# Kernel tuning notes

Hardware: AMD Instinct MI355X
Metric: run time of the kernel (lower is better)

## Reference

```python
import math
import jax, jax.numpy as jnp
import numpy as np

L, D, H, DFF, T, B, BUCKETS = 4, 512, 8, 2048, 256, 8, 32
DH = D // H


def _ln(x, g, b, eps=1e-6):
    m = x.mean(-1, keepdims=True)
    v = ((x - m) ** 2).mean(-1, keepdims=True)
    return (x - m) / jnp.sqrt(v + eps) * g + b


def setup_inputs() -> dict:
    key = jax.random.key(0)
    ki = iter(jax.random.split(key, 32))
    p = lambda shape: jax.random.normal(next(ki), shape, jnp.float32) * 0.02
    inp = {}
    inp['src'] = jax.random.normal(next(ki), (T, B, D), jnp.float32)
    inp['lengths'] = jax.random.randint(next(ki), (B,), 128, T + 1)
    inp['distances'] = jax.random.randint(next(ki), (B, T, T), 0, BUCKETS + 1)
    inp['u'] = jax.random.normal(next(ki), (D,), jnp.float32)
    inp['v'] = jax.random.normal(next(ki), (D,), jnp.float32)
    inp['ln1_g'] = jnp.ones((L, D)); inp['ln1_b'] = jnp.zeros((L, D))
    for nm in ['Wq', 'Wk', 'Wv', 'Wo']:
        inp[nm] = p((L, D, D))
    for nm in ['bq', 'bk', 'bv', 'bo']:
        inp[nm] = jnp.zeros((L, D))
    # learned relative-position embedding table per layer, padding row zeroed
    inp['rel_table'] = p((L, BUCKETS + 1, D)).at[:, BUCKETS, :].set(0.0)
    inp['ffn_ln_g'] = jnp.ones((L, D)); inp['ffn_ln_b'] = jnp.zeros((L, D))
    inp['W1'] = p((L, DFF, D)); inp['b1'] = jnp.zeros((L, DFF))
    inp['W2'] = p((L, D, DFF)); inp['b2'] = jnp.zeros((L, D))
    inp['final_ln_g'] = jnp.ones((D,)); inp['final_ln_b'] = jnp.zeros((D,))
    return inp


def reference(src, lengths, distances, u, v, ln1_g, ln1_b, Wq, bq, Wk, bk, Wv, bv,
              Wo, bo, rel_table, ffn_ln_g, ffn_ln_b, W1, b1, W2, b2,
              final_ln_g, final_ln_b):
    # onmt-style sinusoidal positional encoding with sqrt(d_model) scaling
    pos = jnp.arange(T, dtype=jnp.float32)[:, None]
    div = jnp.exp(jnp.arange(0, D, 2, dtype=jnp.float32) * (-math.log(10000.0) / D))
    pe = jnp.zeros((T, D)).at[:, 0::2].set(jnp.sin(pos * div)).at[:, 1::2].set(jnp.cos(pos * div))
    x = (src * math.sqrt(D) + pe[:, None, :]).transpose(1, 0, 2)  # (B,T,D)
    pad = jnp.arange(T)[None, :] >= lengths[:, None]  # (B,T), True = masked key
    uh = u.reshape(1, H, 1, DH)
    vh = v.reshape(1, H, 1, DH)
    for l in range(L):
        h = _ln(x, ln1_g[l], ln1_b[l])
        def heads(w, b_):
            return (h @ w.T + b_).reshape(B, T, H, DH).transpose(0, 2, 1, 3)
        q = heads(Wq[l], bq[l]) / math.sqrt(DH)  # (B,H,T,DH)
        k = heads(Wk[l], bk[l])
        val = heads(Wv[l], bv[l])
        # content term a_c = (q + u) k^T
        a_c = jnp.einsum('bhqd,bhkd->bhqk', q + uh, k)
        # relative term b_d = (q + v) R^T, R gathered per (query,key) pair
        rel = rel_table[l][distances].reshape(B, T, T, H, DH)  # (B,Q,K,H,DH)
        b_d = jnp.einsum('bhqd,bqkhd->bhqk', q + vh, rel)
        scores = (a_c + b_d).astype(jnp.float32)
        scores = jnp.where(pad[:, None, None, :], -1e18, scores)
        attn = jax.nn.softmax(scores, axis=-1)
        ctx = jnp.einsum('bhqk,bhkd->bhqd', attn, val)
        ctx = ctx.transpose(0, 2, 1, 3).reshape(B, T, D)
        out = ctx @ Wo[l].T + bo[l] + x  # residual (dropout=0)
        # PositionwiseFeedForward: LN -> W1 -> relu -> W2 -> +residual
        h2 = _ln(out, ffn_ln_g[l], ffn_ln_b[l])
        x = jax.nn.relu(h2 @ W1[l].T + b1[l]) @ W2[l].T + b2[l] + out
    x = _ln(x, final_ln_g, final_ln_b)
    return x.transpose(1, 0, 2)  # (T,B,D)
```

## Files before the change

### kernel.cpp

```cpp
#include <hip/hip_runtime.h>
#include <hip/hip_bf16.h>
#include <math.h>

constexpr int L = 4, D = 512, H = 8, DFF = 2048, T = 256, B = 8, BUCKETS = 32;
constexpr int DH = D / H;
constexpr int NT = B * T;
constexpr int QKVLD = 3 * D;

typedef __attribute__((ext_vector_type(8))) short bf16x8;
typedef __attribute__((ext_vector_type(4))) float f32x4;

__device__ __forceinline__ unsigned short f2bf(float f) {
    unsigned int x = __float_as_uint(f);
    return (unsigned short)((x + 0x7fffu + ((x >> 16) & 1u)) >> 16);
}
__device__ __forceinline__ float bf2f(unsigned short u) {
    return __uint_as_float((unsigned int)u << 16);
}

__device__ __forceinline__ void stage16(const unsigned short* g, short* l) {
    __builtin_amdgcn_global_load_lds((const __attribute__((address_space(1))) unsigned int*)g,
                                     (__attribute__((address_space(3))) unsigned int*)l,
                                     16, 0, 0);
}

__global__ __launch_bounds__(256) void embed_kernel(const float* __restrict__ src,
                                                    float* __restrict__ x)
{
    int t = blockIdx.x, tid = threadIdx.x;
    float pe0, pe1;
    {
        int d0 = tid, d1 = tid + 256;
        float dv0 = expf(-(float)(2 * (d0 >> 1)) * (9.210340371976184f / (float)D));
        float dv1 = expf(-(float)(2 * (d1 >> 1)) * (9.210340371976184f / (float)D));
        float a0 = (float)t * dv0, a1 = (float)t * dv1;
        pe0 = (d0 & 1) ? cosf(a0) : sinf(a0);
        pe1 = (d1 & 1) ? cosf(a1) : sinf(a1);
    }
#pragma unroll
    for (int b = 0; b < B; b++) {
        const float* sp = src + ((size_t)t * B + b) * D;
        float* xp = x + ((size_t)(b * T + t)) * D;
        xp[tid]       = sp[tid]       * 22.62741699796952f + pe0;
        xp[tid + 256] = sp[tid + 256] * 22.62741699796952f + pe1;
    }
}

__device__ __forceinline__ void ln_vals(float v0, float v1,
                                        const float* __restrict__ g,
                                        const float* __restrict__ bb,
                                        float* o0, float* o1, int tid)
{
    float s = v0 + v1, q2 = v0 * v0 + v1 * v1;
#pragma unroll
    for (int o = 32; o; o >>= 1) { s += __shfl_xor(s, o); q2 += __shfl_xor(q2, o); }
    __shared__ float rs[4], rq[4];
    int lane = tid & 63, wid = tid >> 6;
    if (lane == 0) { rs[wid] = s; rq[wid] = q2; }
    __syncthreads();
    s = rs[0] + rs[1] + rs[2] + rs[3];
    q2 = rq[0] + rq[1] + rq[2] + rq[3];
    float mean = s * (1.f / (float)D);
    float var = q2 * (1.f / (float)D) - mean * mean;
    float rstd = rsqrtf(var + 1e-6f);
    *o0 = (v0 - mean) * rstd * g[tid] + bb[tid];
    *o1 = (v1 - mean) * rstd * g[tid + 256] + bb[tid + 256];
}

__global__ __launch_bounds__(256) void ln_kernel(const float* __restrict__ x,
                                                 unsigned short* __restrict__ y,
                                                 const float* __restrict__ g,
                                                 const float* __restrict__ bb)
{
    int row = blockIdx.x, tid = threadIdx.x;
    float v0 = x[(size_t)row * D + tid], v1 = x[(size_t)row * D + tid + 256];
    float o0, o1;
    ln_vals(v0, v1, g, bb, &o0, &o1, tid);
    y[(size_t)row * D + tid] = f2bf(o0);
    y[(size_t)row * D + tid + 256] = f2bf(o1);
}

__global__ __launch_bounds__(256) void lnr_kernel(float* __restrict__ X,
                                                  const float* __restrict__ P,
                                                  const float* __restrict__ bias,
                                                  unsigned short* __restrict__ y,
                                                  const float* __restrict__ g,
                                                  const float* __restrict__ bb)
{
    int row = blockIdx.x, tid = threadIdx.x;
    float v0 = X[(size_t)row * D + tid] + bias[tid];
    float v1 = X[(size_t)row * D + tid + 256] + bias[tid + 256];
#pragma unroll
    for (int s = 0; s < 4; s++) {
        v0 += P[((size_t)s * NT + row) * D + tid];
        v1 += P[((size_t)s * NT + row) * D + tid + 256];
    }
    X[(size_t)row * D + tid] = v0;
    X[(size_t)row * D + tid + 256] = v1;
    float o0, o1;
    ln_vals(v0, v1, g, bb, &o0, &o1, tid);
    y[(size_t)row * D + tid] = f2bf(o0);
    y[(size_t)row * D + tid + 256] = f2bf(o1);
}

__global__ __launch_bounds__(256) void final_lnr_kernel(const float* __restrict__ X,
                                                        const float* __restrict__ P,
                                                        const float* __restrict__ bias,
                                                        float* __restrict__ out,
                                                        const float* __restrict__ g,
                                                        const float* __restrict__ bb)
{
    int row = blockIdx.x, tid = threadIdx.x;
    int b = row >> 8, t = row & (T - 1);
    float v0 = X[(size_t)row * D + tid] + bias[tid];
    float v1 = X[(size_t)row * D + tid + 256] + bias[tid + 256];
#pragma unroll
    for (int s = 0; s < 4; s++) {
        v0 += P[((size_t)s * NT + row) * D + tid];
        v1 += P[((size_t)s * NT + row) * D + tid + 256];
    }
    float o0, o1;
    ln_vals(v0, v1, g, bb, &o0, &o1, tid);
    float* op = out + ((size_t)t * B + b) * D;
    op[tid] = o0;
    op[tid + 256] = o1;
}

__global__ __launch_bounds__(256) void convert_all_kernel(
    const float* __restrict__ Wq, const float* __restrict__ Wk, const float* __restrict__ Wv,
    const float* __restrict__ Wo, const float* __restrict__ W1, const float* __restrict__ W2,
    const float* __restrict__ bq, const float* __restrict__ bk, const float* __restrict__ bv,
    const float* __restrict__ rel,
    unsigned short* __restrict__ WQKVb, unsigned short* __restrict__ Wob,
    unsigned short* __restrict__ W1b, unsigned short* __restrict__ W2b,
    unsigned short* __restrict__ relb,
    float* __restrict__ bqkv)
{
    int l = blockIdx.y;
    int g = blockIdx.x * 256 + threadIdx.x;
    const float* src; unsigned short* dst;
    bool zero = false;
    if (g < 98304) {
        int e = g * 8; int piece = e >> 18; int rem = e & 262143;
        src = (piece == 0 ? Wq : piece == 1 ? Wk : Wv) + (size_t)l * 262144 + rem;
        dst = WQKVb + (size_t)l * 786432 + e;
    } else if (g < 131072) {
        int e = (g - 98304) * 8;
        src = Wo + (size_t)l * 262144 + e; dst = Wob + (size_t)l * 262144 + e;
    } else if (g < 262144) {
        int e = (g - 131072) * 8;
        src = W1 + (size_t)l * 1048576 + e; dst = W1b + (size_t)l * 1048576 + e;
    } else if (g < 393216) {
        int e = (g - 262144) * 8;
        src = W2 + (size_t)l * 1048576 + e; dst = W2b + (size_t)l * 1048576 + e;
    } else {
        int e = (g - 393216) * 8;
        int row = e >> 9, cc = e & 511;
        dst = relb + (size_t)l * 24576 + e;
        if (row < BUCKETS + 1) src = rel + ((size_t)l * (BUCKETS + 1) + row) * 512 + cc;
        else { src = nullptr; zero = true; }
    }
    uint4 o;
    if (zero) { o.x = o.y = o.z = o.w = 0u; }
    else {
        float4 x = *(const float4*)src, y = *(const float4*)(src + 4);
        o.x = (unsigned)f2bf(x.x) | ((unsigned)f2bf(x.y) << 16);
        o.y = (unsigned)f2bf(x.z) | ((unsigned)f2bf(x.w) << 16);
        o.z = (unsigned)f2bf(y.x) | ((unsigned)f2bf(y.y) << 16);
        o.w = (unsigned)f2bf(y.z) | ((unsigned)f2bf(y.w) << 16);
    }
    *(uint4*)dst = o;
    if (g < 3 * D) {
        int piece = g >> 9, r2 = g & 511;
        bqkv[l * 1536 + g] = (piece == 0 ? bq : piece == 1 ? bk : bv)[l * 512 + r2];
    }
}

template <bool RELU, bool OUTBF16>
__global__ __launch_bounds__(256) void mgemm_kernel(
    const unsigned short* __restrict__ A,
    const unsigned short* __restrict__ W,
    const float* __restrict__ bias,
    void* __restrict__ Cv,
    int N, int M, int K)
{
    __shared__ short smA[2][128 * 32];
    __shared__ short smB[2][128 * 32];
    int tid = threadIdx.x;
    int bn = blockIdx.y * 128;
    int bm = blockIdx.x * 128;
    const unsigned short* Ab = A + (size_t)bn * K;
    const unsigned short* Wb = W + (size_t)bm * K;

    f32x4 acc[4][4];
#pragma unroll
    for (int i = 0; i < 4; i++)
#pragma unroll
        for (int j = 0; j < 4; j++) acc[i][j] = (f32x4){0.f, 0.f, 0.f, 0.f};

    const int c0 = tid, c1 = tid + 256;
    const int r0 = c0 >> 2, p0 = c0 & 3, l0 = p0 ^ ((r0 >> 1) & 3);
    const int r1 = c1 >> 2, p1 = c1 & 3, l1 = p1 ^ ((r1 >> 1) & 3);

    auto stage = [&](int buf, int k0) {
        stage16(Ab + (size_t)r0 * K + k0 + l0 * 8, &smA[buf][c0 * 8]);
        stage16(Ab + (size_t)r1 * K + k0 + l1 * 8, &smA[buf][c1 * 8]);
        stage16(Wb + (size_t)r0 * K + k0 + l0 * 8, &smB[buf][c0 * 8]);
        stage16(Wb + (size_t)r1 * K + k0 + l1 * 8, &smB[buf][c1 * 8]);
    };

    const int lane = tid & 63;
    const int wv = tid >> 6, wr = wv >> 1, wc = wv & 1;
    int aoff[4], boff[4];
#pragma unroll
    for (int i = 0; i < 4; i++) {
        int ra = wr * 64 + i * 16 + (lane & 15);
        int ca = (lane >> 4) ^ ((ra >> 1) & 3);
        aoff[i] = ra * 32 + ca * 8;
        int rb = wc * 64 + i * 16 + (lane & 15);
        int cb = (lane >> 4) ^ ((rb >> 1) & 3);
        boff[i] = rb * 32 + cb * 8;
    }

    stage(0, 0);
    const int nkt = K >> 5;
    for (int kt = 0; kt < nkt; ++kt) {
        __syncthreads();
        int cur = kt & 1;
        if (kt + 1 < nkt) stage(cur ^ 1, (kt + 1) << 5);
        const short* sa = smA[cur];
        const short* sb = smB[cur];
        bf16x8 af[4], bfr[4];
#pragma unroll
        for (int i = 0; i < 4; i++) af[i] = *(const bf16x8*)(sa + aoff[i]);
#pragma unroll
        for (int j = 0; j < 4; j++) bfr[j] = *(const bf16x8*)(sb + boff[j]);
#pragma unroll
        for (int i = 0; i < 4; i++)
#pragma unroll
            for (int j = 0; j < 4; j++)
                acc[i][j] = __builtin_amdgcn_mfma_f32_16x16x32_bf16(af[i], bfr[j], acc[i][j], 0, 0, 0);
    }

#pragma unroll
    for (int j = 0; j < 4; j++) {
        int col = bm + wc * 64 + j * 16 + (lane & 15);
        float bval = bias[col];
#pragma unroll
        for (int i = 0; i < 4; i++) {
            f32x4 v = acc[i][j];
#pragma unroll
            for (int r = 0; r < 4; r++) {
                int row = bn + wr * 64 + i * 16 + (lane >> 4) * 4 + r;
                float val = v[r] + bval;
                if (RELU) val = fmaxf(val, 0.f);
                if (OUTBF16) ((unsigned short*)Cv)[(size_t)row * M + col] = f2bf(val);
                else         ((float*)Cv)[(size_t)row * M + col] = val;
            }
        }
    }
}

__global__ __launch_bounds__(256) void mgemm_splitk_kernel(
    const unsigned short* __restrict__ A,
    const unsigned short* __restrict__ W,
    float* __restrict__ P,
    int N, int M, int K, int Ksub)
{
    __shared__ short smA[2][128 * 32];
    __shared__ short smB[2][128 * 32];
    int tid = threadIdx.x;
    int s = blockIdx.z;
    int bn = blockIdx.y * 128;
    int bm = blockIdx.x * 128;
    const unsigned short* Ab = A + (size_t)bn * K + s * Ksub;
    const unsigned short* Wb = W + (size_t)bm * K + s * Ksub;

    f32x4 acc[4][4];
#pragma unroll
    for (int i = 0; i < 4; i++)
#pragma unroll
        for (int j = 0; j < 4; j++) acc[i][j] = (f32x4){0.f, 0.f, 0.f, 0.f};

    const int c0 = tid, c1 = tid + 256;
    const int r0 = c0 >> 2, p0 = c0 & 3, l0 = p0 ^ ((r0 >> 1) & 3);
    const int r1 = c1 >> 2, p1 = c1 & 3, l1 = p1 ^ ((r1 >> 1) & 3);

    auto stage = [&](int buf, int k0) {
        stage16(Ab + (size_t)r0 * K + k0 + l0 * 8, &smA[buf][c0 * 8]);
        stage16(Ab + (size_t)r1 * K + k0 + l1 * 8, &smA[buf][c1 * 8]);
        stage16(Wb + (size_t)r0 * K + k0 + l0 * 8, &smB[buf][c0 * 8]);
        stage16(Wb + (size_t)r1 * K + k0 + l1 * 8, &smB[buf][c1 * 8]);
    };

    const int lane = tid & 63;
    const int wv = tid >> 6, wr = wv >> 1, wc = wv & 1;
    int aoff[4], boff[4];
#pragma unroll
    for (int i = 0; i < 4; i++) {
        int ra = wr * 64 + i * 16 + (lane & 15);
        int ca = (lane >> 4) ^ ((ra >> 1) & 3);
        aoff[i] = ra * 32 + ca * 8;
        int rb = wc * 64 + i * 16 + (lane & 15);
        int cb = (lane >> 4) ^ ((rb >> 1) & 3);
        boff[i] = rb * 32 + cb * 8;
    }

    stage(0, 0);
    const int nkt = Ksub >> 5;
    for (int kt = 0; kt < nkt; ++kt) {
        __syncthreads();
        int cur = kt & 1;
        if (kt + 1 < nkt) stage(cur ^ 1, (kt + 1) << 5);
        const short* sa = smA[cur];
        const short* sb = smB[cur];
        bf16x8 af[4], bfr[4];
#pragma unroll
        for (int i = 0; i < 4; i++) af[i] = *(const bf16x8*)(sa + aoff[i]);
#pragma unroll
        for (int j = 0; j < 4; j++) bfr[j] = *(const bf16x8*)(sb + boff[j]);
#pragma unroll
        for (int i = 0; i < 4; i++)
#pragma unroll
            for (int j = 0; j < 4; j++)
                acc[i][j] = __builtin_amdgcn_mfma_f32_16x16x32_bf16(af[i], bfr[j], acc[i][j], 0, 0, 0);
    }

#pragma unroll
    for (int j = 0; j < 4; j++) {
        int col = bm + wc * 64 + j * 16 + (lane & 15);
#pragma unroll
        for (int i = 0; i < 4; i++) {
            f32x4 v = acc[i][j];
#pragma unroll
            for (int r = 0; r < 4; r++) {
                int row = bn + wr * 64 + i * 16 + (lane >> 4) * 4 + r;
                P[((size_t)s * N + row) * M + col] = v[r];
            }
        }
    }
}

__global__ __launch_bounds__(256) void vtrans_kernel(const unsigned short* __restrict__ qkv,
                                                     unsigned short* __restrict__ vt)
{
    __shared__ unsigned short tile[64 * 66];
    int bh = blockIdx.x, b = bh >> 3, h = bh & 7;
    int kc = blockIdx.y * 64;
    int tid = threadIdx.x;
    int r = tid >> 2, c0 = (tid & 3) * 16;
    const unsigned short* rp = qkv + (size_t)(b * T + kc + r) * QKVLD + 2 * D + h * 64 + c0;
    uint4 w0 = *(const uint4*)rp;
    uint4 w1 = *(const uint4*)(rp + 8);
    unsigned short* tp = &tile[r * 66 + c0];
    unsigned int ww[8] = {w0.x, w0.y, w0.z, w0.w, w1.x, w1.y, w1.z, w1.w};
#pragma unroll
    for (int e = 0; e < 8; e++) {
        tp[2 * e]     = (unsigned short)(ww[e] & 0xffffu);
        tp[2 * e + 1] = (unsigned short)(ww[e] >> 16);
    }
    __syncthreads();
    int d = tid >> 2, k0 = (tid & 3) * 16;
    unsigned int outw[8];
#pragma unroll
    for (int i = 0; i < 8; i++) {
        unsigned int lo = tile[(k0 + 2 * i) * 66 + d];
        unsigned int hi = tile[(k0 + 2 * i + 1) * 66 + d];
        outw[i] = lo | (hi << 16);
    }
    unsigned short* op = vt + (size_t)(bh * 64 + d) * 256 + kc + k0;
    *(uint4*)op = *(uint4*)&outw[0];
    *(uint4*)(op + 8) = *(uint4*)&outw[4];
}

__global__ __launch_bounds__(256) void fattn_kernel(
    const unsigned short* __restrict__ qkv,
    const unsigned short* __restrict__ vt,
    const unsigned short* __restrict__ relb,
    const float* __restrict__ uvec,
    const float* __restrict__ vvec,
    const int* __restrict__ dist,
    const int* __restrict__ lengths,
    unsigned short* __restrict__ ctx)
{
    __shared__ unsigned short Ps[4][16][256];
    __shared__ float Qrel[4][16][49];

    int bh = blockIdx.x, b = bh >> 3, h = bh & 7;
    int qi0 = blockIdx.y * 64;
    int tid = threadIdx.x, w = tid >> 6, lane = tid & 63;
    int l15 = lane & 15, g = lane >> 4;
    int qr = qi0 + w * 16;

    const unsigned short* qbase = qkv + (size_t)(b * T + qr + l15) * QKVLD + h * 64 + g * 8;
    bf16x8 qa0 = *(const bf16x8*)(qbase);
    bf16x8 qa1 = *(const bf16x8*)(qbase + 32);

    bf16x8 qu0, qu1;
    {
        const float* up = uvec + h * 64 + g * 8;
        float ua0[8], ua1[8];
        *(float4*)&ua0[0] = *(const float4*)(up);
        *(float4*)&ua0[4] = *(const float4*)(up + 4);
        *(float4*)&ua1[0] = *(const float4*)(up + 32);
        *(float4*)&ua1[4] = *(const float4*)(up + 36);
#pragma unroll
        for (int e = 0; e < 8; e++) {
            qu0[e] = (short)f2bf(0.125f * bf2f((unsigned short)qa0[e]) + ua0[e]);
            qu1[e] = (short)f2bf(0.125f * bf2f((unsigned short)qa1[e]) + ua1[e]);
        }
    }

    {
        const float* vp = vvec + h * 64 + g * 8;
        float va0[8], va1[8];
        *(float4*)&va0[0] = *(const float4*)(vp);
        *(float4*)&va0[4] = *(const float4*)(vp + 4);
        *(float4*)&va1[0] = *(const float4*)(vp + 32);
        *(float4*)&va1[4] = *(const float4*)(vp + 36);
        bf16x8 qh0, qh1;
#pragma unroll
        for (int e = 0; e < 8; e++) {
            qh0[e] = (short)f2bf(0.125f * bf2f((unsigned short)qa0[e]) + va0[e]);
            qh1[e] = (short)f2bf(0.125f * bf2f((unsigned short)qa1[e]) + va1[e]);
        }
        f32x4 qacc[3];
#pragma unroll
        for (int j = 0; j < 3; j++) qacc[j] = (f32x4){0.f, 0.f, 0.f, 0.f};
#pragma unroll
        for (int j = 0; j < 3; j++) {
            const unsigned short* rp = relb + (size_t)(j * 16 + l15) * 512 + h * 64 + g * 8;
            bf16x8 r0 = *(const bf16x8*)(rp);
            bf16x8 r1 = *(const bf16x8*)(rp + 32);
            qacc[j] = __builtin_amdgcn_mfma_f32_16x16x32_bf16(qh0, r0, qacc[j], 0, 0, 0);
            qacc[j] = __builtin_amdgcn_mfma_f32_16x16x32_bf16(qh1, r1, qacc[j], 0, 0, 0);
        }
#pragma unroll
        for (int j = 0; j < 3; j++)
#pragma unroll
            for (int r = 0; r < 4; r++)
                Qrel[w][g * 4 + r][j * 16 + l15] = qacc[j][r];
    }

    f32x4 acc[16];
#pragma unroll
    for (int j = 0; j < 16; j++) acc[j] = (f32x4){0.f, 0.f, 0.f, 0.f};
    const unsigned short* kbase = qkv + (size_t)(b * T) * QKVLD + 512 + h * 64 + g * 8;
#pragma unroll
    for (int j = 0; j < 16; j++) {
        const unsigned short* kp = kbase + (size_t)(j * 16 + l15) * QKVLD;
        bf16x8 k0 = *(const bf16x8*)(kp);
        bf16x8 k1 = *(const bf16x8*)(kp + 32);
        acc[j] = __builtin_amdgcn_mfma_f32_16x16x32_bf16(qu0, k0, acc[j], 0, 0, 0);
        acc[j] = __builtin_amdgcn_mfma_f32_16x16x32_bf16(qu1, k1, acc[j], 0, 0, 0);
    }

    int len = lengths[b];
    float rinv[4];
    const int* db = dist + (size_t)b * T * T;
#pragma unroll
    for (int r = 0; r < 4; r++) {
        int rowloc = g * 4 + r;
        int qrow = qr + rowloc;
        const int* dpr = db + (size_t)qrow * T;
        float m = -3.0e38f;
#pragma unroll
        for (int j = 0; j < 16; j++) {
            int ki = j * 16 + l15;
            int dv = dpr[ki];
            float s = acc[j][r] + Qrel[w][rowloc][dv];
            s = (ki < len) ? s : -1.0e30f;
            acc[j][r] = s;
            m = fmaxf(m, s);
        }
#pragma unroll
        for (int o = 8; o; o >>= 1) m = fmaxf(m, __shfl_xor(m, o));
        float sum = 0.f;
#pragma unroll
        for (int j = 0; j < 16; j++) {
            int ki = j * 16 + l15;
            float p = __expf(acc[j][r] - m);
            sum += p;
            int cph = ((ki >> 3) ^ (rowloc & 7));
            Ps[w][rowloc][cph * 8 + (ki & 7)] = f2bf(p);
        }
#pragma unroll
        for (int o = 8; o; o >>= 1) sum += __shfl_xor(sum, o);
        rinv[r] = 1.0f / sum;
    }

    f32x4 oacc[4];
#pragma unroll
    for (int j = 0; j < 4; j++) oacc[j] = (f32x4){0.f, 0.f, 0.f, 0.f};
    const unsigned short* vtb = vt + (size_t)bh * 64 * 256;
#pragma unroll
    for (int ks = 0; ks < 8; ks++) {
        int c = ks * 4 + g;
        int cph = c ^ (l15 & 7);
        bf16x8 pa = *(const bf16x8*)&Ps[w][l15][cph * 8];
#pragma unroll
        for (int j2 = 0; j2 < 4; j2++) {
            bf16x8 vb = *(const bf16x8*)(vtb + (size_t)(j2 * 16 + l15) * 256 + c * 8);
            oacc[j2] = __builtin_amdgcn_mfma_f32_16x16x32_bf16(pa, vb, oacc[j2], 0, 0, 0);
        }
    }

#pragma unroll
    for (int j2 = 0; j2 < 4; j2++) {
#pragma unroll
        for (int r = 0; r < 4; r++) {
            int qrow = qr + g * 4 + r;
            int dcol = j2 * 16 + l15;
            ctx[(size_t)(b * T + qrow) * D + h * 64 + dcol] = f2bf(oacc[j2][r] * rinv[r]);
        }
    }
}

extern "C" void kernel_launch(void* const* d_in, const int* in_sizes, int n_in,
                              void* d_out, int out_size, void* d_ws, size_t ws_size,
                              hipStream_t stream)
{
    const float* src     = (const float*)d_in[0];
    const int*   lengths = (const int*)d_in[1];
    const int*   dist    = (const int*)d_in[2];
    const float* u       = (const float*)d_in[3];
    const float* v       = (const float*)d_in[4];
    const float* ln1_g   = (const float*)d_in[5];
    const float* ln1_b   = (const float*)d_in[6];
    const float* Wq      = (const float*)d_in[7];
    const float* Wk      = (const float*)d_in[8];
    const float* Wv      = (const float*)d_in[9];
    const float* Wo      = (const float*)d_in[10];
    const float* bq      = (const float*)d_in[11];
    const float* bk      = (const float*)d_in[12];
    const float* bv      = (const float*)d_in[13];
    const float* bo      = (const float*)d_in[14];
    const float* rel     = (const float*)d_in[15];
    const float* fg      = (const float*)d_in[16];
    const float* fb      = (const float*)d_in[17];
    const float* W1      = (const float*)d_in[18];
    const float* b1      = (const float*)d_in[19];
    const float* W2      = (const float*)d_in[20];
    const float* b2      = (const float*)d_in[21];
    const float* flg     = (const float*)d_in[22];
    const float* flb     = (const float*)d_in[23];

    float* ws = (float*)d_ws;
    float*          X     = ws;
    unsigned short* QKVb  = (unsigned short*)(ws + 1048576);
    unsigned short* Hb    = (unsigned short*)(ws + 2621440);
    unsigned short* CTX   = (unsigned short*)(ws + 3145728);
    unsigned short* FF1   = (unsigned short*)(ws + 3670016);
    unsigned short* VT    = (unsigned short*)(ws + 5767168);
    float*          Pbuf  = ws + 6291456;
    unsigned short* WQKVb = (unsigned short*)(ws + 10485760);
    unsigned short* Wob   = (unsigned short*)(ws + 12058624);
    unsigned short* W1b   = (unsigned short*)(ws + 12582912);
    unsigned short* W2b   = (unsigned short*)(ws + 14680064);
    unsigned short* RELb  = (unsigned short*)(ws + 16777216);
    float*          bqkv  = ws + 16826368;

    embed_kernel<<<T, 256, 0, stream>>>(src, X);

    convert_all_kernel<<<dim3(1548, L), 256, 0, stream>>>(
        Wq, Wk, Wv, Wo, W1, W2, bq, bk, bv, rel,
        WQKVb, Wob, W1b, W2b, RELb, bqkv);

    for (int l = 0; l < L; l++) {
        const unsigned short* wqkv = WQKVb + (size_t)l * 786432;
        const unsigned short* wob  = Wob   + (size_t)l * 262144;
        const unsigned short* w1b  = W1b   + (size_t)l * 1048576;
        const unsigned short* w2b  = W2b   + (size_t)l * 1048576;
        const unsigned short* relb = RELb  + (size_t)l * 24576;
        const float*          bql  = bqkv  + (size_t)l * 1536;

        if (l == 0)
            ln_kernel<<<NT, 256, 0, stream>>>(X, Hb, ln1_g, ln1_b);
        else
            lnr_kernel<<<NT, 256, 0, stream>>>(X, Pbuf, b2 + (size_t)(l - 1) * D,
                                               Hb, ln1_g + l * D, ln1_b + l * D);

        mgemm_kernel<false, true><<<dim3(12, 16), 256, 0, stream>>>(
            Hb, wqkv, bql, QKVb, NT, QKVLD, D);

        vtrans_kernel<<<dim3(64, 4), 256, 0, stream>>>(QKVb, VT);

        fattn_kernel<<<dim3(B * H, T / 64), 256, 0, stream>>>(
            QKVb, VT, relb, u, v, dist, lengths, CTX);

        mgemm_splitk_kernel<<<dim3(4, 16, 4), 256, 0, stream>>>(
            CTX, wob, Pbuf, NT, D, D, D / 4);

        lnr_kernel<<<NT, 256, 0, stream>>>(X, Pbuf, bo + (size_t)l * D,
                                           Hb, fg + l * D, fb + l * D);

        mgemm_kernel<true, true><<<dim3(16, 16), 256, 0, stream>>>(
            Hb, w1b, b1 + (size_t)l * DFF, FF1, NT, DFF, D);

        mgemm_splitk_kernel<<<dim3(4, 16, 4), 256, 0, stream>>>(
            FF1, w2b, Pbuf, NT, D, DFF, DFF / 4);
    }

    final_lnr_kernel<<<NT, 256, 0, stream>>>(X, Pbuf, b2 + (size_t)(L - 1) * D,
                                             (float*)d_out, flg, flb);
}
```

Measured before the change: 521.8 us.

## Fuse embedding into first LayerNorm and write transposed V from QKV GEMM epilogue

Merges the positional-embedding kernel into the first LayerNorm so the embedded activations are computed, stored and normalised in one pass, dropping a kernel launch and a reread of X. The QKV GEMM epilogue also writes the V columns directly in the transposed per-head layout used by attention, which removes the separate vtrans kernel and its extra read of QKV. In exchange the embed kernel now recomputes sin/cos per row and the GEMM epilogue performs scattered 8-byte transposed stores. The split-K store index was also changed from N to NT, which gives the same value at the existing call sites.

```diff
diff --git a/kernel.cpp b/kernel.cpp
--- a/kernel.cpp
+++ b/kernel.cpp
@@ -24,32 +24,10 @@
                                      16, 0, 0);
 }
 
-__global__ __launch_bounds__(256) void embed_kernel(const float* __restrict__ src,
-                                                    float* __restrict__ x)
-{
-    int t = blockIdx.x, tid = threadIdx.x;
-    float pe0, pe1;
-    {
-        int d0 = tid, d1 = tid + 256;
-        float dv0 = expf(-(float)(2 * (d0 >> 1)) * (9.210340371976184f / (float)D));
-        float dv1 = expf(-(float)(2 * (d1 >> 1)) * (9.210340371976184f / (float)D));
-        float a0 = (float)t * dv0, a1 = (float)t * dv1;
-        pe0 = (d0 & 1) ? cosf(a0) : sinf(a0);
-        pe1 = (d1 & 1) ? cosf(a1) : sinf(a1);
-    }
-#pragma unroll
-    for (int b = 0; b < B; b++) {
-        const float* sp = src + ((size_t)t * B + b) * D;
-        float* xp = x + ((size_t)(b * T + t)) * D;
-        xp[tid]       = sp[tid]       * 22.62741699796952f + pe0;
-        xp[tid + 256] = sp[tid + 256] * 22.62741699796952f + pe1;
-    }
-}
-
-__device__ __forceinline__ void ln_vals(float v0, float v1,
-                                        const float* __restrict__ g,
-                                        const float* __restrict__ bb,
-                                        float* o0, float* o1, int tid)
+__device__ __forceinline__ void ln_vals_k(float v0, float v1,
+                                          const float* __restrict__ g,
+                                          const float* __restrict__ bb,
+                                          float* o0, float* o1, int tid)
 {
     float s = v0 + v1, q2 = v0 * v0 + v1 * v1;
 #pragma unroll
@@ -67,17 +45,29 @@
     *o1 = (v1 - mean) * rstd * g[tid + 256] + bb[tid + 256];
 }
 
-__global__ __launch_bounds__(256) void ln_kernel(const float* __restrict__ x,
-                                                 unsigned short* __restrict__ y,
-                                                 const float* __restrict__ g,
-                                                 const float* __restrict__ bb)
+__global__ __launch_bounds__(256) void embed_ln_kernel(const float* __restrict__ src,
+                                                       float* __restrict__ X,
+                                                       unsigned short* __restrict__ Hb,
+                                                       const float* __restrict__ g,
+                                                       const float* __restrict__ bb)
 {
     int row = blockIdx.x, tid = threadIdx.x;
-    float v0 = x[(size_t)row * D + tid], v1 = x[(size_t)row * D + tid + 256];
+    int b = row >> 8, t = row & (T - 1);
+    int d0 = tid, d1 = tid + 256;
+    float dv0 = expf(-(float)(2 * (d0 >> 1)) * (9.210340371976184f / (float)D));
+    float dv1 = expf(-(float)(2 * (d1 >> 1)) * (9.210340371976184f / (float)D));
+    float a0 = (float)t * dv0, a1 = (float)t * dv1;
+    float pe0 = (d0 & 1) ? cosf(a0) : sinf(a0);
+    float pe1 = (d1 & 1) ? cosf(a1) : sinf(a1);
+    const float* sp = src + ((size_t)t * B + b) * D;
+    float v0 = sp[d0] * 22.62741699796952f + pe0;
+    float v1 = sp[d1] * 22.62741699796952f + pe1;
+    X[(size_t)row * D + d0] = v0;
+    X[(size_t)row * D + d1] = v1;
     float o0, o1;
-    ln_vals(v0, v1, g, bb, &o0, &o1, tid);
-    y[(size_t)row * D + tid] = f2bf(o0);
-    y[(size_t)row * D + tid + 256] = f2bf(o1);
+    ln_vals_k(v0, v1, g, bb, &o0, &o1, tid);
+    Hb[(size_t)row * D + d0] = f2bf(o0);
+    Hb[(size_t)row * D + d1] = f2bf(o1);
 }
 
 __global__ __launch_bounds__(256) void lnr_kernel(float* __restrict__ X,
@@ -98,7 +88,7 @@
     X[(size_t)row * D + tid] = v0;
     X[(size_t)row * D + tid + 256] = v1;
     float o0, o1;
-    ln_vals(v0, v1, g, bb, &o0, &o1, tid);
+    ln_vals_k(v0, v1, g, bb, &o0, &o1, tid);
     y[(size_t)row * D + tid] = f2bf(o0);
     y[(size_t)row * D + tid + 256] = f2bf(o1);
 }
@@ -120,7 +110,7 @@
         v1 += P[((size_t)s * NT + row) * D + tid + 256];
     }
     float o0, o1;
-    ln_vals(v0, v1, g, bb, &o0, &o1, tid);
+    ln_vals_k(v0, v1, g, bb, &o0, &o1, tid);
     float* op = out + ((size_t)t * B + b) * D;
     op[tid] = o0;
     op[tid + 256] = o1;
@@ -176,12 +166,13 @@
     }
 }
 
-template <bool RELU, bool OUTBF16>
+template <bool RELU, bool OUTBF16, bool VTOUT>
 __global__ __launch_bounds__(256) void mgemm_kernel(
     const unsigned short* __restrict__ A,
     const unsigned short* __restrict__ W,
     const float* __restrict__ bias,
     void* __restrict__ Cv,
+    unsigned short* __restrict__ vt,
     int N, int M, int K)
 {
     __shared__ short smA[2][128 * 32];
@@ -249,13 +240,24 @@
 #pragma unroll
         for (int i = 0; i < 4; i++) {
             f32x4 v = acc[i][j];
+            int row0 = bn + wr * 64 + i * 16 + (lane >> 4) * 4;
+            unsigned short ob[4];
 #pragma unroll
             for (int r = 0; r < 4; r++) {
-                int row = bn + wr * 64 + i * 16 + (lane >> 4) * 4 + r;
                 float val = v[r] + bval;
                 if (RELU) val = fmaxf(val, 0.f);
-                if (OUTBF16) ((unsigned short*)Cv)[(size_t)row * M + col] = f2bf(val);
-                else         ((float*)Cv)[(size_t)row * M + col] = val;
+                unsigned short bfv = f2bf(val);
+                ob[r] = bfv;
+                if (OUTBF16) ((unsigned short*)Cv)[(size_t)(row0 + r) * M + col] = bfv;
+                else         ((float*)Cv)[(size_t)(row0 + r) * M + col] = val;
+            }
+            if (VTOUT && col >= 1024) {
+                int d = col - 1024;
+                int b = row0 >> 8, ki = row0 & (T - 1);
+                uint2 pk;
+                pk.x = (unsigned)ob[0] | ((unsigned)ob[1] << 16);
+                pk.y = (unsigned)ob[2] | ((unsigned)ob[3] << 16);
+                *(uint2*)(vt + ((size_t)(b * H + (d >> 6)) * 64 + (d & 63)) * 256 + ki) = pk;
             }
         }
     }
@@ -335,42 +337,10 @@
 #pragma unroll
             for (int r = 0; r < 4; r++) {
                 int row = bn + wr * 64 + i * 16 + (lane >> 4) * 4 + r;
-                P[((size_t)s * N + row) * M + col] = v[r];
+                P[((size_t)s * NT + row) * M + col] = v[r];
             }
         }
     }
-}
-
-__global__ __launch_bounds__(256) void vtrans_kernel(const unsigned short* __restrict__ qkv,
-                                                     unsigned short* __restrict__ vt)
-{
-    __shared__ unsigned short tile[64 * 66];
-    int bh = blockIdx.x, b = bh >> 3, h = bh & 7;
-    int kc = blockIdx.y * 64;
-    int tid = threadIdx.x;
-    int r = tid >> 2, c0 = (tid & 3) * 16;
-    const unsigned short* rp = qkv + (size_t)(b * T + kc + r) * QKVLD + 2 * D + h * 64 + c0;
-    uint4 w0 = *(const uint4*)rp;
-    uint4 w1 = *(const uint4*)(rp + 8);
-    unsigned short* tp = &tile[r * 66 + c0];
-    unsigned int ww[8] = {w0.x, w0.y, w0.z, w0.w, w1.x, w1.y, w1.z, w1.w};
-#pragma unroll
-    for (int e = 0; e < 8; e++) {
-        tp[2 * e]     = (unsigned short)(ww[e] & 0xffffu);
-        tp[2 * e + 1] = (unsigned short)(ww[e] >> 16);
-    }
-    __syncthreads();
-    int d = tid >> 2, k0 = (tid & 3) * 16;
-    unsigned int outw[8];
-#pragma unroll
-    for (int i = 0; i < 8; i++) {
-        unsigned int lo = tile[(k0 + 2 * i) * 66 + d];
-        unsigned int hi = tile[(k0 + 2 * i + 1) * 66 + d];
-        outw[i] = lo | (hi << 16);
-    }
-    unsigned short* op = vt + (size_t)(bh * 64 + d) * 256 + kc + k0;
-    *(uint4*)op = *(uint4*)&outw[0];
-    *(uint4*)(op + 8) = *(uint4*)&outw[4];
 }
 
 __global__ __launch_bounds__(256) void fattn_kernel(
@@ -430,10 +400,10 @@
 #pragma unroll
         for (int j = 0; j < 3; j++) {
             const unsigned short* rp = relb + (size_t)(j * 16 + l15) * 512 + h * 64 + g * 8;
-            bf16x8 r0 = *(const bf16x8*)(rp);
-            bf16x8 r1 = *(const bf16x8*)(rp + 32);
-            qacc[j] = __builtin_amdgcn_mfma_f32_16x16x32_bf16(qh0, r0, qacc[j], 0, 0, 0);
-            qacc[j] = __builtin_amdgcn_mfma_f32_16x16x32_bf16(qh1, r1, qacc[j], 0, 0, 0);
+            bf16x8 rr0 = *(const bf16x8*)(rp);
+            bf16x8 rr1 = *(const bf16x8*)(rp + 32);
+            qacc[j] = __builtin_amdgcn_mfma_f32_16x16x32_bf16(qh0, rr0, qacc[j], 0, 0, 0);
+            qacc[j] = __builtin_amdgcn_mfma_f32_16x16x32_bf16(qh1, rr1, qacc[j], 0, 0, 0);
         }
 #pragma unroll
         for (int j = 0; j < 3; j++)
@@ -560,11 +530,11 @@
     unsigned short* RELb  = (unsigned short*)(ws + 16777216);
     float*          bqkv  = ws + 16826368;
 
-    embed_kernel<<<T, 256, 0, stream>>>(src, X);
-
     convert_all_kernel<<<dim3(1548, L), 256, 0, stream>>>(
         Wq, Wk, Wv, Wo, W1, W2, bq, bk, bv, rel,
         WQKVb, Wob, W1b, W2b, RELb, bqkv);
+
+    embed_ln_kernel<<<NT, 256, 0, stream>>>(src, X, Hb, ln1_g, ln1_b);
 
     for (int l = 0; l < L; l++) {
         const unsigned short* wqkv = WQKVb + (size_t)l * 786432;
@@ -574,16 +544,12 @@
         const unsigned short* relb = RELb  + (size_t)l * 24576;
         const float*          bql  = bqkv  + (size_t)l * 1536;
 
-        if (l == 0)
-            ln_kernel<<<NT, 256, 0, stream>>>(X, Hb, ln1_g, ln1_b);
-        else
+        if (l > 0)
             lnr_kernel<<<NT, 256, 0, stream>>>(X, Pbuf, b2 + (size_t)(l - 1) * D,
                                                Hb, ln1_g + l * D, ln1_b + l * D);
 
-        mgemm_kernel<false, true><<<dim3(12, 16), 256, 0, stream>>>(
-            Hb, wqkv, bql, QKVb, NT, QKVLD, D);
-
-        vtrans_kernel<<<dim3(64, 4), 256, 0, stream>>>(QKVb, VT);
+        mgemm_kernel<false, true, true><<<dim3(12, 16), 256, 0, stream>>>(
+            Hb, wqkv, bql, QKVb, VT, NT, QKVLD, D);
 
         fattn_kernel<<<dim3(B * H, T / 64), 256, 0, stream>>>(
             QKVb, VT, relb, u, v, dist, lengths, CTX);
@@ -594,8 +560,8 @@
         lnr_kernel<<<NT, 256, 0, stream>>>(X, Pbuf, bo + (size_t)l * D,
                                            Hb, fg + l * D, fb + l * D);
 
-        mgemm_kernel<true, true><<<dim3(16, 16), 256, 0, stream>>>(
-            Hb, w1b, b1 + (size_t)l * DFF, FF1, NT, DFF, D);
+        mgemm_kernel<true, true, false><<<dim3(16, 16), 256, 0, stream>>>(
+            Hb, w1b, b1 + (size_t)l * DFF, FF1, nullptr, NT, DFF, D);
 
         mgemm_splitk_kernel<<<dim3(4, 16, 4), 256, 0, stream>>>(
             FF1, w2b, Pbuf, NT, D, DFF, DFF / 4);
```

Measured after the change: 518.9 us. No clear change (-0.6%).
